# Kernel tuning notes

Hardware: AMD Instinct MI355X
Metric: run time of the kernel (lower is better)

The kernel has to match this reference:

```python
import jax, jax.numpy as jnp
import numpy as np

SCALE = 8.0  # sqrt(head_dim=64)
B, H, S, D = 2, 16, 2048, 64


def setup_inputs() -> dict:
    key = jax.random.key(0)
    kq, kk, kv = jax.random.split(key, 3)
    query = jax.random.normal(kq, (B, H, S, D), dtype=jnp.float32)
    key_t = jax.random.normal(kk, (B, H, S, D), dtype=jnp.float32)
    value = jax.random.normal(kv, (B, H, S, D), dtype=jnp.float32)
    # causal target mask (B, 1, S, S); 0 = masked
    mask = jnp.broadcast_to(jnp.tril(jnp.ones((S, S), dtype=jnp.int32)), (B, 1, S, S))
    return {"query": query, "key": key_t, "value": value, "mask": mask}


def reference(query, key, value, mask):
    # scores: (B, H, S, S)
    scores = jnp.einsum("bhqd,bhkd->bhqk", query, key) / SCALE
    scores = jnp.where(mask == 0, -jnp.inf, scores)
    attn = jax.nn.softmax(scores, axis=-1)  # dropout_rate=0.0 -> identity
    return jnp.einsum("bhqk,bhkd->bhqd", attn, value)
```

## Files before the change

### kernel.cpp

```cpp
#include <hip/hip_runtime.h>
#include <hip/hip_bf16.h>


#define S_ 2048
#define D_ 64
#define NBH 32

typedef __bf16 bf16x8 __attribute__((ext_vector_type(8)));
typedef float f32x4 __attribute__((ext_vector_type(4)));
typedef unsigned short u16x4 __attribute__((ext_vector_type(4)));
typedef unsigned short u16x8 __attribute__((ext_vector_type(8)));

static __device__ __forceinline__ unsigned short bfb(float f) {
    return __builtin_bit_cast(unsigned short, (__bf16)f);
}

__global__ __launch_bounds__(256)
void prep_kv(const float* __restrict__ K, const float* __restrict__ V,
             unsigned short* __restrict__ Kbf, unsigned short* __restrict__ Vt) {
    const int bh = blockIdx.x >> 5;
    const int kvbase = (blockIdx.x & 31) << 6;

    const float* Ks = K + (size_t)bh * S_ * D_ + (size_t)kvbase * D_;
    unsigned short* Kd = Kbf + (size_t)bh * S_ * D_ + (size_t)kvbase * D_;
    #pragma unroll
    for (int i = 0; i < 4; ++i) {
        const int p = i * 256 + threadIdx.x;
        float4 x = reinterpret_cast<const float4*>(Ks)[p];
        u16x4 o = { bfb(x.x), bfb(x.y), bfb(x.z), bfb(x.w) };
        reinterpret_cast<u16x4*>(Kd)[p] = o;
    }

    __shared__ float Vl[64][65];
    const float* Vb = V + (size_t)bh * S_ * D_ + (size_t)kvbase * D_;
    #pragma unroll
    for (int i = 0; i < 4; ++i) {
        const int flat = i * 1024 + threadIdx.x * 4;
        const int kv = flat >> 6, d = flat & 63;
        float4 x = *reinterpret_cast<const float4*>(Vb + kv * D_ + d);
        Vl[kv][d] = x.x; Vl[kv][d + 1] = x.y; Vl[kv][d + 2] = x.z; Vl[kv][d + 3] = x.w;
    }
    __syncthreads();
    unsigned short* Vo = Vt + (size_t)bh * D_ * S_;
    #pragma unroll
    for (int i = 0; i < 2; ++i) {
        const int p = i * 256 + threadIdx.x;
        const int d = p >> 3, c = p & 7;
        u16x8 o;
        #pragma unroll
        for (int j = 0; j < 8; ++j) o[j] = bfb(Vl[c * 8 + j][d]);
        *reinterpret_cast<u16x8*>(Vo + d * S_ + kvbase + c * 8) = o;
    }
}

__global__ __launch_bounds__(256)
void attn_fwd3(const float* __restrict__ Q, const unsigned short* __restrict__ Kbf,
               const unsigned short* __restrict__ Vtbf, float* __restrict__ O) {
    const int tid  = threadIdx.x;
    const int wave = tid >> 6;
    const int lane = tid & 63;
    const int lg   = lane >> 4;
    const int lr   = lane & 15;

    const int wg = blockIdx.x;
    const int bh = wg & 31;
    const int pr = wg >> 5;

    const float*          Qb = Q    + (size_t)bh * S_ * D_;
    const unsigned short* Kg = Kbf  + (size_t)bh * S_ * D_;
    const unsigned short* Vg = Vtbf + (size_t)bh * D_ * S_;
    float*                Ob = O    + (size_t)bh * S_ * D_;

    __shared__ __align__(16) unsigned short Kl[2][4096];
    __shared__ __align__(16) unsigned short Vl[2][4096];
    __shared__ unsigned short Pl[4][16][72];

    bf16x8 ones;
    #pragma unroll
    for (int i = 0; i < 8; ++i) ones[i] = (__bf16)1.0f;

    auto stage = [&](int buf, int t) {
        #pragma unroll
        for (int i = 0; i < 2; ++i) {
            const int p   = wave * 128 + i * 64 + lane;
            const int row = p >> 3, c = p & 7;
            const int sc  = c ^ (row & 7);
            const unsigned short* gk = Kg + (size_t)(t * 64 + row) * 64 + sc * 8;
            __builtin_amdgcn_global_load_lds(
                (const __attribute__((address_space(1))) void*)gk,
                (__attribute__((address_space(3))) void*)&Kl[buf][p * 8], 16, 0, 0);
            const unsigned short* gv = Vg + (size_t)row * S_ + t * 64 + sc * 8;
            __builtin_amdgcn_global_load_lds(
                (const __attribute__((address_space(1))) void*)gv,
                (__attribute__((address_space(3))) void*)&Vl[buf][p * 8], 16, 0, 0);
        }
    };

    const float qscale = 0.18033688011112042f;

    auto run_pass = [&](int q0) {
        bf16x8 qa[2];
        {
            const int qrow = q0 + wave * 16 + lr;
            #pragma unroll
            for (int kt = 0; kt < 2; ++kt) {
                const float* src = Qb + qrow * D_ + kt * 32 + lg * 8;
                float4 x = *reinterpret_cast<const float4*>(src);
                float4 y = *reinterpret_cast<const float4*>(src + 4);
                union { unsigned short u[8]; bf16x8 v; } pk;
                pk.u[0] = bfb(x.x * qscale); pk.u[1] = bfb(x.y * qscale);
                pk.u[2] = bfb(x.z * qscale); pk.u[3] = bfb(x.w * qscale);
                pk.u[4] = bfb(y.x * qscale); pk.u[5] = bfb(y.y * qscale);
                pk.u[6] = bfb(y.z * qscale); pk.u[7] = bfb(y.w * qscale);
                qa[kt] = pk.v;
            }
        }

        f32x4 oacc[4];
        #pragma unroll
        for (int i = 0; i < 4; ++i) oacc[i] = {0.f, 0.f, 0.f, 0.f};
        float m_[4], l_[4];
        #pragma unroll
        for (int r = 0; r < 4; ++r) { m_[r] = -__builtin_inff(); l_[r] = 0.f; }

        const int nkv = (q0 >> 6) + 1;
        stage(0, 0);
        __syncthreads();

        for (int t = 0; t < nkv; ++t) {
            if (t + 1 < nkv) stage((t + 1) & 1, t + 1);
            const unsigned short* Kb_ = Kl[t & 1];
            const unsigned short* Vb_ = Vl[t & 1];
            const int kvbase = t << 6;

            f32x4 sacc[4];
            __builtin_amdgcn_s_setprio(1);
            #pragma unroll
            for (int kvt = 0; kvt < 4; ++kvt) {
                sacc[kvt] = {0.f, 0.f, 0.f, 0.f};
                #pragma unroll
                for (int kt = 0; kt < 2; ++kt) {
                    bf16x8 kb = *reinterpret_cast<const bf16x8*>(
                        &Kb_[((kvt * 16 + lr) * 8 + ((kt * 4 + lg) ^ (lr & 7))) * 8]);
                    sacc[kvt] = __builtin_amdgcn_mfma_f32_16x16x32_bf16(qa[kt], kb, sacc[kvt], 0, 0, 0);
                }
            }
            __builtin_amdgcn_s_setprio(0);

            if (t == nkv - 1) {
                #pragma unroll
                for (int kvt = 0; kvt < 4; ++kvt) {
                    const int kvg = kvbase + kvt * 16 + lr;
                    #pragma unroll
                    for (int r = 0; r < 4; ++r) {
                        const int qg = q0 + wave * 16 + lg * 4 + r;
                        if (kvg > qg) sacc[kvt][r] = -__builtin_inff();
                    }
                }
            }

            float pm[4];
            bool resc = false;
            #pragma unroll
            for (int r = 0; r < 4; ++r) {
                float v = fmaxf(fmaxf(sacc[0][r], sacc[1][r]), fmaxf(sacc[2][r], sacc[3][r]));
                #pragma unroll
                for (int off = 1; off < 16; off <<= 1)
                    v = fmaxf(v, __shfl_xor(v, off, 16));
                pm[r] = v;
                resc = resc || (v > m_[r] + 8.0f);
            }
            if (__any((int)resc)) {
                #pragma unroll
                for (int r = 0; r < 4; ++r) {
                    const float mn = fmaxf(m_[r], pm[r]);
                    const float al = __builtin_amdgcn_exp2f(m_[r] - mn);
                    m_[r] = mn;
                    l_[r] *= al;
                    #pragma unroll
                    for (int dt = 0; dt < 4; ++dt) oacc[dt][r] *= al;
                }
            }
            #pragma unroll
            for (int kvt = 0; kvt < 4; ++kvt)
                #pragma unroll
                for (int r = 0; r < 4; ++r)
                    sacc[kvt][r] = __builtin_amdgcn_exp2f(sacc[kvt][r] - m_[r]);

            #pragma unroll
            for (int kvt = 0; kvt < 4; ++kvt)
                #pragma unroll
                for (int r = 0; r < 4; ++r)
                    Pl[wave][lg * 4 + r][kvt * 16 + lr] = bfb(sacc[kvt][r]);

            bf16x8 pa0 = *reinterpret_cast<const bf16x8*>(&Pl[wave][lr][lg * 8]);
            bf16x8 pa1 = *reinterpret_cast<const bf16x8*>(&Pl[wave][lr][32 + lg * 8]);

            f32x4 ssum = {0.f, 0.f, 0.f, 0.f};
            __builtin_amdgcn_s_setprio(1);
            #pragma unroll
            for (int dt = 0; dt < 4; ++dt) {
                bf16x8 vb0 = *reinterpret_cast<const bf16x8*>(
                    &Vb_[((dt * 16 + lr) * 8 + ((0 * 4 + lg) ^ (lr & 7))) * 8]);
                oacc[dt] = __builtin_amdgcn_mfma_f32_16x16x32_bf16(pa0, vb0, oacc[dt], 0, 0, 0);
                bf16x8 vb1 = *reinterpret_cast<const bf16x8*>(
                    &Vb_[((dt * 16 + lr) * 8 + ((1 * 4 + lg) ^ (lr & 7))) * 8]);
                oacc[dt] = __builtin_amdgcn_mfma_f32_16x16x32_bf16(pa1, vb1, oacc[dt], 0, 0, 0);
            }
            ssum = __builtin_amdgcn_mfma_f32_16x16x32_bf16(pa0, ones, ssum, 0, 0, 0);
            ssum = __builtin_amdgcn_mfma_f32_16x16x32_bf16(pa1, ones, ssum, 0, 0, 0);
            __builtin_amdgcn_s_setprio(0);

            #pragma unroll
            for (int r = 0; r < 4; ++r) l_[r] += ssum[r];

            __syncthreads();
        }

        #pragma unroll
        for (int r = 0; r < 4; ++r) {
            const int qrow = q0 + wave * 16 + lg * 4 + r;
            const float inv = 1.0f / l_[r];
            #pragma unroll
            for (int dt = 0; dt < 4; ++dt)
                Ob[(size_t)qrow * D_ + dt * 16 + lr] = oacc[dt][r] * inv;
        }
    };

    run_pass((31 - pr) << 6);
    __syncthreads();
    run_pass(pr << 6);
}

extern "C" void kernel_launch(void* const* d_in, const int* in_sizes, int n_in,
                              void* d_out, int out_size, void* d_ws, size_t ws_size,
                              hipStream_t stream) {
    const float* Q = (const float*)d_in[0];
    const float* K = (const float*)d_in[1];
    const float* V = (const float*)d_in[2];
    float* O = (float*)d_out;

    unsigned short* Kbf = (unsigned short*)d_ws;
    unsigned short* Vt  = Kbf + (size_t)NBH * S_ * D_;

    hipLaunchKernelGGL(prep_kv,   dim3(1024), dim3(256), 0, stream, K, V, Kbf, Vt);
    hipLaunchKernelGGL(attn_fwd3, dim3(512),  dim3(256), 0, stream, Q, Kbf, Vt, O);
}
```

Measured before the change: 159.2 us.

## Rewrite attention kernel with 32x32 MFMA, register-resident P and per-block tiles

Replaces the 16x16x32 MFMA flash-attention kernel with one built on 32x32x16 bf16 MFMA. It computes S transposed (K as the A operand) so each lane holds a query column, which removes the per-row 16-lane shuffle reductions. P is passed to the PV MFMA through register shuffles instead of an LDS round-trip, and the row sum is computed in registers rather than with MFMAs against a ones vector. Work is split into 1024 blocks of 128 threads (2 waves × 32 query rows) with launch_bounds(128,2), dropping the paired long/short causal pass per block. This gives up the explicit load balancing of that pairing and leaves heavier register use per lane.

```diff
diff --git a/kernel.cpp b/kernel.cpp
--- a/kernel.cpp
+++ b/kernel.cpp
@@ -7,12 +7,17 @@
 #define NBH 32
 
 typedef __bf16 bf16x8 __attribute__((ext_vector_type(8)));
-typedef float f32x4 __attribute__((ext_vector_type(4)));
+typedef float f32x16 __attribute__((ext_vector_type(16)));
 typedef unsigned short u16x4 __attribute__((ext_vector_type(4)));
 typedef unsigned short u16x8 __attribute__((ext_vector_type(8)));
+typedef unsigned int u32;
+typedef u32 u32x4 __attribute__((ext_vector_type(4)));
 
 static __device__ __forceinline__ unsigned short bfb(float f) {
     return __builtin_bit_cast(unsigned short, (__bf16)f);
+}
+static __device__ __forceinline__ u32 pk2(float lo, float hi) {
+    return (u32)bfb(lo) | ((u32)bfb(hi) << 16);
 }
 
 __global__ __launch_bounds__(256)
@@ -53,183 +58,176 @@
     }
 }
 
-__global__ __launch_bounds__(256)
-void attn_fwd3(const float* __restrict__ Q, const unsigned short* __restrict__ Kbf,
+#define MFMA32(a, b, c) __builtin_amdgcn_mfma_f32_32x32x16_bf16((a), (b), (c), 0, 0, 0)
+
+__global__ __launch_bounds__(128, 2)
+void attn_fwd4(const float* __restrict__ Q, const unsigned short* __restrict__ Kbf,
                const unsigned short* __restrict__ Vtbf, float* __restrict__ O) {
     const int tid  = threadIdx.x;
-    const int wave = tid >> 6;
+    const int wq   = tid >> 6;
     const int lane = tid & 63;
-    const int lg   = lane >> 4;
-    const int lr   = lane & 15;
-
-    const int wg = blockIdx.x;
-    const int bh = wg & 31;
-    const int pr = wg >> 5;
-
-    const float*          Qb = Q    + (size_t)bh * S_ * D_;
+    const int lq   = lane & 31;
+    const int hi   = lane >> 5;
+
+    const int bid = blockIdx.x;
+    const int qb  = 31 - (bid >> 5);
+    const int bh  = bid & 31;
+    const int q0  = qb * 64 + wq * 32;
+
     const unsigned short* Kg = Kbf  + (size_t)bh * S_ * D_;
     const unsigned short* Vg = Vtbf + (size_t)bh * D_ * S_;
-    float*                Ob = O    + (size_t)bh * S_ * D_;
 
     __shared__ __align__(16) unsigned short Kl[2][4096];
     __shared__ __align__(16) unsigned short Vl[2][4096];
-    __shared__ unsigned short Pl[4][16][72];
-
-    bf16x8 ones;
-    #pragma unroll
-    for (int i = 0; i < 8; ++i) ones[i] = (__bf16)1.0f;
-
+
+    const float qscale = 0.18033688011112042f;
+    bf16x8 qf[4];
+    {
+        const float* qsrc = Q + ((size_t)bh * S_ + q0 + lq) * D_;
+        #pragma unroll
+        for (int ks = 0; ks < 4; ++ks) {
+            const float* p = qsrc + ks * 16 + hi * 8;
+            float4 x = *reinterpret_cast<const float4*>(p);
+            float4 y = *reinterpret_cast<const float4*>(p + 4);
+            union { unsigned short u[8]; bf16x8 v; } t;
+            t.u[0] = bfb(x.x * qscale); t.u[1] = bfb(x.y * qscale);
+            t.u[2] = bfb(x.z * qscale); t.u[3] = bfb(x.w * qscale);
+            t.u[4] = bfb(y.x * qscale); t.u[5] = bfb(y.y * qscale);
+            t.u[6] = bfb(y.z * qscale); t.u[7] = bfb(y.w * qscale);
+            qf[ks] = t.v;
+        }
+    }
+
+    const unsigned short* kSrc[4];
+    const unsigned short* vSrc[4];
+    #pragma unroll
+    for (int j = 0; j < 4; ++j) {
+        const int p = j * 128 + tid, row = p >> 3;
+        const int sc = (p & 7) ^ (row & 7);
+        kSrc[j] = Kg + row * 64 + sc * 8;
+        vSrc[j] = Vg + (size_t)row * S_ + sc * 8;
+    }
     auto stage = [&](int buf, int t) {
         #pragma unroll
-        for (int i = 0; i < 2; ++i) {
-            const int p   = wave * 128 + i * 64 + lane;
-            const int row = p >> 3, c = p & 7;
-            const int sc  = c ^ (row & 7);
-            const unsigned short* gk = Kg + (size_t)(t * 64 + row) * 64 + sc * 8;
+        for (int j = 0; j < 4; ++j) {
+            const int p = j * 128 + tid;
             __builtin_amdgcn_global_load_lds(
-                (const __attribute__((address_space(1))) void*)gk,
+                (const __attribute__((address_space(1))) void*)(kSrc[j] + t * 4096),
                 (__attribute__((address_space(3))) void*)&Kl[buf][p * 8], 16, 0, 0);
-            const unsigned short* gv = Vg + (size_t)row * S_ + t * 64 + sc * 8;
             __builtin_amdgcn_global_load_lds(
-                (const __attribute__((address_space(1))) void*)gv,
+                (const __attribute__((address_space(1))) void*)(vSrc[j] + t * 64),
                 (__attribute__((address_space(3))) void*)&Vl[buf][p * 8], 16, 0, 0);
         }
     };
 
-    const float qscale = 0.18033688011112042f;
-
-    auto run_pass = [&](int q0) {
-        bf16x8 qa[2];
+    f32x16 oa0, oa1;
+    #pragma unroll
+    for (int r = 0; r < 16; ++r) { oa0[r] = 0.f; oa1[r] = 0.f; }
+    float m_ = -__builtin_inff(), l_ = 0.f;
+
+    const int nkv = qb + 1;
+    stage(0, 0);
+    __syncthreads();
+
+    for (int t = 0; t < nkv; ++t) {
+        if (t + 1 < nkv) stage((t + 1) & 1, t + 1);
+        const unsigned short* Kb_ = Kl[t & 1];
+        const unsigned short* Vb_ = Vl[t & 1];
+
+        f32x16 s0, s1;
+        #pragma unroll
+        for (int r = 0; r < 16; ++r) { s0[r] = 0.f; s1[r] = 0.f; }
+        __builtin_amdgcn_s_setprio(1);
+        #pragma unroll
+        for (int ks = 0; ks < 4; ++ks) {
+            const int cc = 2 * ks + hi;
+            bf16x8 k0 = *reinterpret_cast<const bf16x8*>(
+                &Kb_[((lq)*8      + (cc ^ (lq & 7))) * 8]);
+            bf16x8 k1 = *reinterpret_cast<const bf16x8*>(
+                &Kb_[((32 + lq)*8 + (cc ^ (lq & 7))) * 8]);
+            s0 = MFMA32(k0, qf[ks], s0);
+            s1 = MFMA32(k1, qf[ks], s1);
+        }
+        __builtin_amdgcn_s_setprio(0);
+
+        if (t == nkv - 1) {
+            const int qg = q0 + lq - t * 64;
+            #pragma unroll
+            for (int r = 0; r < 16; ++r) {
+                const int kv0 = (r & 3) + 8 * (r >> 2) + 4 * hi;
+                if (kv0 > qg)      s0[r] = -__builtin_inff();
+                if (kv0 + 32 > qg) s1[r] = -__builtin_inff();
+            }
+        }
+
+        float v = s0[0];
+        #pragma unroll
+        for (int r = 1; r < 16; ++r) v = fmaxf(v, s0[r]);
+        #pragma unroll
+        for (int r = 0; r < 16; ++r) v = fmaxf(v, s1[r]);
+        v = fmaxf(v, __shfl_xor(v, 32));
+
+        if (__any(v > m_ + 8.0f ? 1 : 0)) {
+            const float mn = fmaxf(m_, v);
+            const float al = __builtin_amdgcn_exp2f(m_ - mn);
+            m_ = mn;
+            l_ *= al;
+            #pragma unroll
+            for (int r = 0; r < 16; ++r) { oa0[r] *= al; oa1[r] *= al; }
+        }
+        #pragma unroll
+        for (int r = 0; r < 16; ++r) {
+            s0[r] = __builtin_amdgcn_exp2f(s0[r] - m_);
+            s1[r] = __builtin_amdgcn_exp2f(s1[r] - m_);
+        }
         {
-            const int qrow = q0 + wave * 16 + lr;
+            float rs = 0.f;
             #pragma unroll
-            for (int kt = 0; kt < 2; ++kt) {
-                const float* src = Qb + qrow * D_ + kt * 32 + lg * 8;
-                float4 x = *reinterpret_cast<const float4*>(src);
-                float4 y = *reinterpret_cast<const float4*>(src + 4);
-                union { unsigned short u[8]; bf16x8 v; } pk;
-                pk.u[0] = bfb(x.x * qscale); pk.u[1] = bfb(x.y * qscale);
-                pk.u[2] = bfb(x.z * qscale); pk.u[3] = bfb(x.w * qscale);
-                pk.u[4] = bfb(y.x * qscale); pk.u[5] = bfb(y.y * qscale);
-                pk.u[6] = bfb(y.z * qscale); pk.u[7] = bfb(y.w * qscale);
-                qa[kt] = pk.v;
-            }
-        }
-
-        f32x4 oacc[4];
-        #pragma unroll
-        for (int i = 0; i < 4; ++i) oacc[i] = {0.f, 0.f, 0.f, 0.f};
-        float m_[4], l_[4];
-        #pragma unroll
-        for (int r = 0; r < 4; ++r) { m_[r] = -__builtin_inff(); l_[r] = 0.f; }
-
-        const int nkv = (q0 >> 6) + 1;
-        stage(0, 0);
+            for (int r = 0; r < 16; ++r) rs += s0[r] + s1[r];
+            rs += __shfl_xor(rs, 32);
+            l_ += rs;
+        }
+
+        u32 c0[4][2], c1[4][2];
+        #pragma unroll
+        for (int tq = 0; tq < 4; ++tq) {
+            c0[tq][0] = pk2(s0[4*tq+0], s0[4*tq+1]);
+            c0[tq][1] = pk2(s0[4*tq+2], s0[4*tq+3]);
+            c1[tq][0] = pk2(s1[4*tq+0], s1[4*tq+1]);
+            c1[tq][1] = pk2(s1[4*tq+2], s1[4*tq+3]);
+        }
+
+        __builtin_amdgcn_s_setprio(1);
+#define PVSTEP(KS, C) { \
+            const int tl = (2*(KS)) & 3; \
+            u32 a0 = C[tl][0], a1 = C[tl][1], b0 = C[tl+1][0], b1 = C[tl+1][1]; \
+            u32 pa0 = __shfl_xor(a0, 32), pa1 = __shfl_xor(a1, 32); \
+            u32 pb0 = __shfl_xor(b0, 32), pb1 = __shfl_xor(b1, 32); \
+            u32x4 w = { hi ? pb0 : a0, hi ? pb1 : a1, hi ? b0 : pa0, hi ? b1 : pa1 }; \
+            bf16x8 pf = __builtin_bit_cast(bf16x8, w); \
+            const int cc = 2*(KS) + hi; \
+            bf16x8 v0 = *reinterpret_cast<const bf16x8*>( \
+                &Vb_[((lq)*8      + (cc ^ (lq & 7))) * 8]); \
+            bf16x8 v1 = *reinterpret_cast<const bf16x8*>( \
+                &Vb_[((32 + lq)*8 + (cc ^ (lq & 7))) * 8]); \
+            oa0 = MFMA32(v0, pf, oa0); \
+            oa1 = MFMA32(v1, pf, oa1); }
+        PVSTEP(0, c0) PVSTEP(1, c0) PVSTEP(2, c1) PVSTEP(3, c1)
+#undef PVSTEP
+        __builtin_amdgcn_s_setprio(0);
+
         __syncthreads();
-
-        for (int t = 0; t < nkv; ++t) {
-            if (t + 1 < nkv) stage((t + 1) & 1, t + 1);
-            const unsigned short* Kb_ = Kl[t & 1];
-            const unsigned short* Vb_ = Vl[t & 1];
-            const int kvbase = t << 6;
-
-            f32x4 sacc[4];
-            __builtin_amdgcn_s_setprio(1);
-            #pragma unroll
-            for (int kvt = 0; kvt < 4; ++kvt) {
-                sacc[kvt] = {0.f, 0.f, 0.f, 0.f};
-                #pragma unroll
-                for (int kt = 0; kt < 2; ++kt) {
-                    bf16x8 kb = *reinterpret_cast<const bf16x8*>(
-                        &Kb_[((kvt * 16 + lr) * 8 + ((kt * 4 + lg) ^ (lr & 7))) * 8]);
-                    sacc[kvt] = __builtin_amdgcn_mfma_f32_16x16x32_bf16(qa[kt], kb, sacc[kvt], 0, 0, 0);
-                }
-            }
-            __builtin_amdgcn_s_setprio(0);
-
-            if (t == nkv - 1) {
-                #pragma unroll
-                for (int kvt = 0; kvt < 4; ++kvt) {
-                    const int kvg = kvbase + kvt * 16 + lr;
-                    #pragma unroll
-                    for (int r = 0; r < 4; ++r) {
-                        const int qg = q0 + wave * 16 + lg * 4 + r;
-                        if (kvg > qg) sacc[kvt][r] = -__builtin_inff();
-                    }
-                }
-            }
-
-            float pm[4];
-            bool resc = false;
-            #pragma unroll
-            for (int r = 0; r < 4; ++r) {
-                float v = fmaxf(fmaxf(sacc[0][r], sacc[1][r]), fmaxf(sacc[2][r], sacc[3][r]));
-                #pragma unroll
-                for (int off = 1; off < 16; off <<= 1)
-                    v = fmaxf(v, __shfl_xor(v, off, 16));
-                pm[r] = v;
-                resc = resc || (v > m_[r] + 8.0f);
-            }
-            if (__any((int)resc)) {
-                #pragma unroll
-                for (int r = 0; r < 4; ++r) {
-                    const float mn = fmaxf(m_[r], pm[r]);
-                    const float al = __builtin_amdgcn_exp2f(m_[r] - mn);
-                    m_[r] = mn;
-                    l_[r] *= al;
-                    #pragma unroll
-                    for (int dt = 0; dt < 4; ++dt) oacc[dt][r] *= al;
-                }
-            }
-            #pragma unroll
-            for (int kvt = 0; kvt < 4; ++kvt)
-                #pragma unroll
-                for (int r = 0; r < 4; ++r)
-                    sacc[kvt][r] = __builtin_amdgcn_exp2f(sacc[kvt][r] - m_[r]);
-
-            #pragma unroll
-            for (int kvt = 0; kvt < 4; ++kvt)
-                #pragma unroll
-                for (int r = 0; r < 4; ++r)
-                    Pl[wave][lg * 4 + r][kvt * 16 + lr] = bfb(sacc[kvt][r]);
-
-            bf16x8 pa0 = *reinterpret_cast<const bf16x8*>(&Pl[wave][lr][lg * 8]);
-            bf16x8 pa1 = *reinterpret_cast<const bf16x8*>(&Pl[wave][lr][32 + lg * 8]);
-
-            f32x4 ssum = {0.f, 0.f, 0.f, 0.f};
-            __builtin_amdgcn_s_setprio(1);
-            #pragma unroll
-            for (int dt = 0; dt < 4; ++dt) {
-                bf16x8 vb0 = *reinterpret_cast<const bf16x8*>(
-                    &Vb_[((dt * 16 + lr) * 8 + ((0 * 4 + lg) ^ (lr & 7))) * 8]);
-                oacc[dt] = __builtin_amdgcn_mfma_f32_16x16x32_bf16(pa0, vb0, oacc[dt], 0, 0, 0);
-                bf16x8 vb1 = *reinterpret_cast<const bf16x8*>(
-                    &Vb_[((dt * 16 + lr) * 8 + ((1 * 4 + lg) ^ (lr & 7))) * 8]);
-                oacc[dt] = __builtin_amdgcn_mfma_f32_16x16x32_bf16(pa1, vb1, oacc[dt], 0, 0, 0);
-            }
-            ssum = __builtin_amdgcn_mfma_f32_16x16x32_bf16(pa0, ones, ssum, 0, 0, 0);
-            ssum = __builtin_amdgcn_mfma_f32_16x16x32_bf16(pa1, ones, ssum, 0, 0, 0);
-            __builtin_amdgcn_s_setprio(0);
-
-            #pragma unroll
-            for (int r = 0; r < 4; ++r) l_[r] += ssum[r];
-
-            __syncthreads();
-        }
-
-        #pragma unroll
-        for (int r = 0; r < 4; ++r) {
-            const int qrow = q0 + wave * 16 + lg * 4 + r;
-            const float inv = 1.0f / l_[r];
-            #pragma unroll
-            for (int dt = 0; dt < 4; ++dt)
-                Ob[(size_t)qrow * D_ + dt * 16 + lr] = oacc[dt][r] * inv;
-        }
-    };
-
-    run_pass((31 - pr) << 6);
-    __syncthreads();
-    run_pass(pr << 6);
+    }
+
+    const float inv = 1.0f / l_;
+    float* Ob = O + ((size_t)bh * S_ + q0 + lq) * D_;
+    #pragma unroll
+    for (int g = 0; g < 4; ++g) {
+        float4 o0 = { oa0[4*g+0]*inv, oa0[4*g+1]*inv, oa0[4*g+2]*inv, oa0[4*g+3]*inv };
+        *reinterpret_cast<float4*>(&Ob[8*g + 4*hi]) = o0;
+        float4 o1 = { oa1[4*g+0]*inv, oa1[4*g+1]*inv, oa1[4*g+2]*inv, oa1[4*g+3]*inv };
+        *reinterpret_cast<float4*>(&Ob[32 + 8*g + 4*hi]) = o1;
+    }
 }
 
 extern "C" void kernel_launch(void* const* d_in, const int* in_sizes, int n_in,
@@ -244,5 +242,5 @@
     unsigned short* Vt  = Kbf + (size_t)NBH * S_ * D_;
 
     hipLaunchKernelGGL(prep_kv,   dim3(1024), dim3(256), 0, stream, K, V, Kbf, Vt);
-    hipLaunchKernelGGL(attn_fwd3, dim3(512),  dim3(256), 0, stream, Q, Kbf, Vt, O);
-}
+    hipLaunchKernelGGL(attn_fwd4, dim3(1024), dim3(128), 0, stream, Q, Kbf, Vt, O);
+}
```

Measured after the change: 153.9 us. 1.03x faster.
